# Performance work log

Hardware: AMD Instinct MI355X
Metric: run time of the kernel (lower is better)

The kernel has to match this reference:

```python
import jax, jax.numpy as jnp
import numpy as np

N_NODES = 100000
N_EDGES = 1600000
IN_FEATS = 128
OUT_FEATS = 48


def setup_inputs() -> dict:
    key = jax.random.key(0)
    ks = jax.random.split(key, 6)
    features = jax.random.normal(ks[0], (N_NODES, IN_FEATS), dtype=jnp.float32)
    # xavier_uniform for W.weight [out, in]
    lim_w = float(np.sqrt(6.0 / (IN_FEATS + OUT_FEATS)))
    W_w = jax.random.uniform(ks[1], (OUT_FEATS, IN_FEATS), dtype=jnp.float32, minval=-lim_w, maxval=lim_w)
    W_b = jnp.zeros((OUT_FEATS,), dtype=jnp.float32)
    # xavier_uniform for attn_w [2*out, 1]
    lim_a = float(np.sqrt(6.0 / (2 * OUT_FEATS + 1)))
    attn_w = jax.random.uniform(ks[2], (2 * OUT_FEATS, 1), dtype=jnp.float32, minval=-lim_a, maxval=lim_a)
    attn_b = jnp.zeros((1,), dtype=jnp.float32)
    src = jax.random.randint(ks[3], (N_EDGES,), 0, N_NODES, dtype=jnp.int32)
    dst = jax.random.randint(ks[4], (N_EDGES,), 0, N_NODES, dtype=jnp.int32)
    return {"features": features, "W_w": W_w, "W_b": W_b,
            "attn_w": attn_w, "attn_b": attn_b, "src": src, "dst": dst}


def reference(features, W_w, W_b, attn_w, attn_b, src, dst):
    n = features.shape[0]
    d = W_w.shape[0]
    # h = W(features)  [N, d]
    h = features @ W_w.T + W_b
    # cat([h[src], h[dst]]) @ attn_w == h[src] @ w_src + h[dst] @ w_dst
    w_src = attn_w[:d, 0]   # [d]
    w_dst = attn_w[d:, 0]   # [d]
    s_src = h @ w_src       # [N]
    s_dst = h @ w_dst       # [N]
    e = s_src[src] + s_dst[dst] + attn_b[0]            # [E]
    e = jax.nn.leaky_relu(e, negative_slope=0.2)
    # edge softmax grouped by destination node
    m = jax.ops.segment_max(e, dst, num_segments=n)     # [N]
    ex = jnp.exp(e - m[dst])                            # [E]
    denom = jax.ops.segment_sum(ex, dst, num_segments=n)  # [N]
    alpha = ex / denom[dst]                             # [E]
    # weighted scatter-sum: out[v] = sum_{(u,v) in E} alpha * h[u]
    msgs = h[src] * alpha[:, None]                      # [E, d]
    out = jax.ops.segment_sum(msgs, dst, num_segments=n)  # [N, d]
    return out
```

## Files before the change

kernel.cpp:

```cpp
#include <hip/hip_runtime.h>

#define NFEAT 128
#define DOUT 48
#define BSH 6
#define BNODES 64
#define PCAP 192
#define BCAP (PCAP * 8)
#define EPT 16
#define NBMAX 1568

typedef __attribute__((ext_vector_type(8))) short bf16x8;
typedef __attribute__((ext_vector_type(4))) float f32x4;

__device__ __forceinline__ float bf_lo(unsigned u) { return __uint_as_float(u << 16); }
__device__ __forceinline__ float bf_hi(unsigned u) { return __uint_as_float(u & 0xFFFF0000u); }
__device__ __forceinline__ unsigned bf_pack(float a, float b) {
    unsigned ua = __float_as_uint(a), ub = __float_as_uint(b);
    ua = (ua + 0x7FFFu + ((ua >> 16) & 1u)) >> 16;
    ub = (ub + 0x7FFFu + ((ub >> 16) & 1u)) & 0xFFFF0000u;
    return ua | ub;
}

__device__ __forceinline__ void split2(float x, short& hi, short& lo) {
    unsigned u = __float_as_uint(x);
    unsigned h = u & 0xFFFF0000u;
    hi = (short)(h >> 16);
    float r = x - __uint_as_float(h);
    unsigned v = __float_as_uint(r);
    lo = (short)((v + 0x7FFFu + ((v >> 16) & 1u)) >> 16);
}

__global__ __launch_bounds__(256) void k_proj(
    const float* __restrict__ feat, const float* __restrict__ Ww,
    const float* __restrict__ Wb, const float* __restrict__ attn_w,
    unsigned* __restrict__ hbf, float* __restrict__ s_src, float* __restrict__ s_dst,
    int n)
{
    __shared__ float hb[128][49];

    int tid  = threadIdx.x;
    int lane = tid & 63;
    int wv   = tid >> 6;
    int g    = lane >> 4;
    int r16  = lane & 15;

    int mbase = blockIdx.x * 128 + wv * 32;
    int na0 = mbase + r16;       if (na0 >= n) na0 = n - 1;
    int na1 = mbase + 16 + r16;  if (na1 >= n) na1 = n - 1;

    const float* fA0 = feat + (size_t)na0 * NFEAT + g * 4;
    const float* fA1 = feat + (size_t)na1 * NFEAT + g * 4;
    const float* wB  = Ww + (size_t)r16 * NFEAT + g * 4;

    f32x4 acc[2][3];
#pragma unroll
    for (int mt = 0; mt < 2; ++mt)
#pragma unroll
        for (int nt = 0; nt < 3; ++nt)
            acc[mt][nt] = (f32x4){0.f, 0.f, 0.f, 0.f};

#pragma unroll
    for (int ks = 0; ks < 4; ++ks) {
        f32x4 ra[4], rb[6];
        ra[0] = *(const f32x4*)(fA0 + ks * 32);
        ra[1] = *(const f32x4*)(fA0 + ks * 32 + 16);
        ra[2] = *(const f32x4*)(fA1 + ks * 32);
        ra[3] = *(const f32x4*)(fA1 + ks * 32 + 16);
        rb[0] = *(const f32x4*)(wB + ks * 32);
        rb[1] = *(const f32x4*)(wB + ks * 32 + 16);
        rb[2] = *(const f32x4*)(wB + 16 * NFEAT + ks * 32);
        rb[3] = *(const f32x4*)(wB + 16 * NFEAT + ks * 32 + 16);
        rb[4] = *(const f32x4*)(wB + 32 * NFEAT + ks * 32);
        rb[5] = *(const f32x4*)(wB + 32 * NFEAT + ks * 32 + 16);

        bf16x8 Ah[2], Al[2], Bh[3], Bl[3];
#pragma unroll
        for (int t = 0; t < 2; ++t) {
#pragma unroll
            for (int i = 0; i < 4; ++i) {
                short h, l;
                split2(ra[2 * t][i], h, l);     Ah[t][i] = h;     Al[t][i] = l;
                split2(ra[2 * t + 1][i], h, l); Ah[t][i + 4] = h; Al[t][i + 4] = l;
            }
        }
#pragma unroll
        for (int t = 0; t < 3; ++t) {
#pragma unroll
            for (int i = 0; i < 4; ++i) {
                short h, l;
                split2(rb[2 * t][i], h, l);     Bh[t][i] = h;     Bl[t][i] = l;
                split2(rb[2 * t + 1][i], h, l); Bh[t][i + 4] = h; Bl[t][i + 4] = l;
            }
        }
#pragma unroll
        for (int mt = 0; mt < 2; ++mt)
#pragma unroll
            for (int nt = 0; nt < 3; ++nt) {
                acc[mt][nt] = __builtin_amdgcn_mfma_f32_16x16x32_bf16(Ah[mt], Bh[nt], acc[mt][nt], 0, 0, 0);
                acc[mt][nt] = __builtin_amdgcn_mfma_f32_16x16x32_bf16(Al[mt], Bh[nt], acc[mt][nt], 0, 0, 0);
                acc[mt][nt] = __builtin_amdgcn_mfma_f32_16x16x32_bf16(Ah[mt], Bl[nt], acc[mt][nt], 0, 0, 0);
            }
    }

#pragma unroll
    for (int mt = 0; mt < 2; ++mt)
#pragma unroll
        for (int nt = 0; nt < 3; ++nt)
#pragma unroll
            for (int rr = 0; rr < 4; ++rr)
                hb[wv * 32 + mt * 16 + 4 * g + rr][nt * 16 + r16] = acc[mt][nt][rr];
    __syncthreads();

    int node = tid >> 1, part = tid & 1, jb = part * 24;
    int gn = blockIdx.x * 128 + node;
    float v[24];
    float ss = 0.f, sd = 0.f;
#pragma unroll
    for (int j = 0; j < 24; ++j) {
        float x = hb[node][jb + j] + Wb[jb + j];
        v[j] = x;
        ss = fmaf(x, attn_w[jb + j], ss);
        sd = fmaf(x, attn_w[DOUT + jb + j], sd);
    }
    ss += __shfl_xor(ss, 1, 64);
    sd += __shfl_xor(sd, 1, 64);

    if (gn < n) {
        uint4* hp = (uint4*)(hbf + (size_t)gn * 24 + part * 12);
#pragma unroll
        for (int q = 0; q < 3; ++q) {
            uint4 u;
            u.x = bf_pack(v[8 * q + 0], v[8 * q + 1]);
            u.y = bf_pack(v[8 * q + 2], v[8 * q + 3]);
            u.z = bf_pack(v[8 * q + 4], v[8 * q + 5]);
            u.w = bf_pack(v[8 * q + 6], v[8 * q + 7]);
            hp[q] = u;
        }
        if (part == 0) {
            s_src[gn] = ss;
            s_dst[gn] = sd;
        }
    }
}

__global__ __launch_bounds__(256) void k_bin(
    const int4* __restrict__ src4, const int4* __restrict__ dst4,
    const float* __restrict__ s_src, const float* __restrict__ s_dst,
    const float* __restrict__ attn_b,
    int* __restrict__ cursor, int2* __restrict__ ents, int nE, int NB)
{
    __shared__ int hist[NBMAX];
    __shared__ int bas[NBMAX];

    int tid = threadIdx.x;
    int cls = blockIdx.x & 7;
    long long e0 = (long long)blockIdx.x * 4096 + (long long)tid * EPT;

    for (int t = tid; t < NB; t += 256) hist[t] = 0;
    __syncthreads();

    int s[EPT], d[EPT];
    bool any = (e0 < nE);
#pragma unroll
    for (int q = 0; q < EPT / 4; ++q) {
        int4 sv = any ? src4[e0 / 4 + q] : make_int4(0, 0, 0, 0);
        int4 dv = any ? dst4[e0 / 4 + q] : make_int4(0, 0, 0, 0);
        s[4 * q + 0] = sv.x; s[4 * q + 1] = sv.y; s[4 * q + 2] = sv.z; s[4 * q + 3] = sv.w;
        d[4 * q + 0] = dv.x; d[4 * q + 1] = dv.y; d[4 * q + 2] = dv.z; d[4 * q + 3] = dv.w;
    }

    float vs[EPT], vd[EPT];
#pragma unroll
    for (int u = 0; u < EPT; ++u) vs[u] = s_src[s[u]];
#pragma unroll
    for (int u = 0; u < EPT; ++u) vd[u] = s_dst[d[u]];

    int rank[EPT];
#pragma unroll
    for (int u = 0; u < EPT; ++u)
        rank[u] = (e0 + u < nE) ? atomicAdd(&hist[d[u] >> BSH], 1) : 0;
    __syncthreads();

    for (int t = tid; t < NB; t += 256) {
        int c = hist[t];
        if (c > 0) bas[t] = atomicAdd(cursor + cls * NB + t, c);
    }
    __syncthreads();

    float ab = attn_b[0];
#pragma unroll
    for (int u = 0; u < EPT; ++u) {
        if (e0 + u < nE) {
            float v = vs[u] + vd[u] + ab;
            v = (v > 0.f) ? v : 0.2f * v;
            float x = __expf(v);
            int bkt = d[u] >> BSH;
            int slot = bas[bkt] + rank[u];
            if (slot < PCAP)
                ents[(size_t)bkt * BCAP + cls * PCAP + slot] =
                    make_int2(s[u] | ((d[u] & (BNODES - 1)) << 17), __float_as_int(x));
        }
    }
}

__global__ __launch_bounds__(256) void k_aggb(
    const unsigned* __restrict__ hbf, const int* __restrict__ cursor,
    const int2* __restrict__ ents, float* __restrict__ out, int n, int NB)
{
    __shared__ int2 se[BCAP];
    __shared__ unsigned short sidx[BCAP];
    __shared__ int c1[BNODES], c2[BNODES], lrp[BNODES + 1];
    __shared__ int cp[9];

    int b = blockIdx.x;
    int tid = threadIdx.x;

    if (tid < BNODES) { c1[tid] = 0; c2[tid] = 0; }
    __syncthreads();
    if (tid == 0) {
        int r = 0;
        for (int c = 0; c < 8; ++c) {
            cp[c] = r;
            r += min(cursor[c * NB + b], PCAP);
        }
        cp[8] = r;
    }
    __syncthreads();
    int total = cp[8];

    for (int i = tid; i < total; i += 256) {
        int c = 0;
        while (i >= cp[c + 1]) ++c;
        int2 v = ents[(size_t)b * BCAP + c * PCAP + (i - cp[c])];
        se[i] = v;
        atomicAdd(&c1[((unsigned)v.x) >> 17], 1);
    }
    __syncthreads();

    if (tid < BNODES) {
        int v = c1[tid];
        int p = v;
#pragma unroll
        for (int o = 1; o < 64; o <<= 1) {
            int u = __shfl_up(p, o, 64);
            if (tid >= o) p += u;
        }
        lrp[tid] = p - v;
        if (tid == BNODES - 1) lrp[BNODES] = p;
    }
    __syncthreads();

    for (int i = tid; i < total; i += 256) {
        int dl = ((unsigned)se[i].x) >> 17;
        int pos = lrp[dl] + atomicAdd(&c2[dl], 1);
        sidx[pos] = (unsigned short)i;
    }
    __syncthreads();

    int wave = tid >> 6, lane = tid & 63;
    int g = lane >> 3, sub = lane & 7;
    for (int dl = wave; dl < BNODES; dl += 4) {
        int node = (b << BSH) + dl;
        if (node >= n) break;
        int st = lrp[dl], en = lrp[dl + 1];
        float a0 = 0.f, a1 = 0.f, a2 = 0.f, a3 = 0.f, a4 = 0.f, a5 = 0.f, den = 0.f;
        for (int k = st + g; k < en; k += 8) {
            int2 ed = se[sidx[k]];
            float x = __int_as_float(ed.y);
            den += x;
            const unsigned* hr = hbf + (size_t)(ed.x & 0x1FFFF) * 24 + sub * 3;
            unsigned u0 = hr[0], u1 = hr[1], u2 = hr[2];
            a0 = fmaf(x, bf_lo(u0), a0);
            a1 = fmaf(x, bf_hi(u0), a1);
            a2 = fmaf(x, bf_lo(u1), a2);
            a3 = fmaf(x, bf_hi(u1), a3);
            a4 = fmaf(x, bf_lo(u2), a4);
            a5 = fmaf(x, bf_hi(u2), a5);
        }
#pragma unroll
        for (int o = 8; o <= 32; o <<= 1) {
            a0  += __shfl_xor(a0, o, 64);
            a1  += __shfl_xor(a1, o, 64);
            a2  += __shfl_xor(a2, o, 64);
            a3  += __shfl_xor(a3, o, 64);
            a4  += __shfl_xor(a4, o, 64);
            a5  += __shfl_xor(a5, o, 64);
            den += __shfl_xor(den, o, 64);
        }
        if (lane < 8) {
            float inv = (en > st) ? 1.f / den : 0.f;
            float* op = out + (size_t)node * DOUT + sub * 6;
            op[0] = a0 * inv;
            op[1] = a1 * inv;
            op[2] = a2 * inv;
            op[3] = a3 * inv;
            op[4] = a4 * inv;
            op[5] = a5 * inv;
        }
    }
}

extern "C" void kernel_launch(void* const* d_in, const int* in_sizes, int n_in,
                              void* d_out, int out_size, void* d_ws, size_t ws_size,
                              hipStream_t stream) {
    const float* feat   = (const float*)d_in[0];
    const float* Ww     = (const float*)d_in[1];
    const float* Wb     = (const float*)d_in[2];
    const float* attn_w = (const float*)d_in[3];
    const float* attn_b = (const float*)d_in[4];
    const int*   src    = (const int*)d_in[5];
    const int*   dst    = (const int*)d_in[6];

    int n  = in_sizes[0] / NFEAT;
    int nE = in_sizes[5];
    int NB = (n + BNODES - 1) / BNODES;
    int N8 = NB * 8;
    float* out = (float*)d_out;

    unsigned* hbf  = (unsigned*)d_ws;
    float* s_src   = (float*)(hbf + (size_t)n * 24);
    float* s_dst   = s_src + n;
    int*   cursor  = (int*)(s_dst + n);
    int2*  ents    = (int2*)(cursor + N8);

    hipMemsetAsync(cursor, 0, (size_t)N8 * sizeof(int), stream);

    int NBp = (n + 127) / 128;
    k_proj<<<NBp, 256, 0, stream>>>(feat, Ww, Wb, attn_w, hbf, s_src, s_dst, n);
    int nbb = (nE + 4095) / 4096;
    k_bin<<<nbb, 256, 0, stream>>>((const int4*)src, (const int4*)dst,
                                   s_src, s_dst, attn_b, cursor, ents, nE, NB);
    k_aggb<<<NB, 256, 0, stream>>>(hbf, cursor, ents, out, n, NB);
}
```

Before: 193.3 us.

## Pad bf16 h rows to 128B, widen aggregation block, sort edges directly

Pads each bf16 node row in the projected feature buffer from 96 to 128 bytes so every gathered row starts on a cache-line boundary. The aggregation kernel moves to 512 threads with 8 waves sharing the 64 destination nodes, and replaces the computed prefix over class counts with a shuffle scan. It stores sorted edge records directly instead of an index indirection, and unrolls the gather loop by two for more loads in flight. In exchange it uses more workspace and LDS (a second int2 array), which may lower occupancy.

```diff
diff --git a/kernel.cpp b/kernel.cpp
--- a/kernel.cpp
+++ b/kernel.cpp
@@ -8,6 +8,7 @@
 #define BCAP (PCAP * 8)
 #define EPT 16
 #define NBMAX 1568
+#define HSTRIDE 32
 
 typedef __attribute__((ext_vector_type(8))) short bf16x8;
 typedef __attribute__((ext_vector_type(4))) float f32x4;
@@ -126,7 +127,7 @@
     sd += __shfl_xor(sd, 1, 64);
 
     if (gn < n) {
-        uint4* hp = (uint4*)(hbf + (size_t)gn * 24 + part * 12);
+        uint4* hp = (uint4*)(hbf + (size_t)gn * HSTRIDE + part * 12);
 #pragma unroll
         for (int q = 0; q < 3; ++q) {
             uint4 u;
@@ -203,12 +204,12 @@
     }
 }
 
-__global__ __launch_bounds__(256) void k_aggb(
+__global__ __launch_bounds__(512) void k_aggb(
     const unsigned* __restrict__ hbf, const int* __restrict__ cursor,
     const int2* __restrict__ ents, float* __restrict__ out, int n, int NB)
 {
     __shared__ int2 se[BCAP];
-    __shared__ unsigned short sidx[BCAP];
+    __shared__ int2 sse[BCAP];
     __shared__ int c1[BNODES], c2[BNODES], lrp[BNODES + 1];
     __shared__ int cp[9];
 
@@ -216,19 +217,21 @@
     int tid = threadIdx.x;
 
     if (tid < BNODES) { c1[tid] = 0; c2[tid] = 0; }
-    __syncthreads();
-    if (tid == 0) {
-        int r = 0;
-        for (int c = 0; c < 8; ++c) {
-            cp[c] = r;
-            r += min(cursor[c * NB + b], PCAP);
-        }
-        cp[8] = r;
+    if (tid < 8) {
+        int c = min(cursor[tid * NB + b], PCAP);
+        int p = c;
+#pragma unroll
+        for (int o = 1; o < 8; o <<= 1) {
+            int u = __shfl_up(p, o, 64);
+            if (tid >= o) p += u;
+        }
+        cp[tid + 1] = p;
+        if (tid == 0) cp[0] = 0;
     }
     __syncthreads();
     int total = cp[8];
 
-    for (int i = tid; i < total; i += 256) {
+    for (int i = tid; i < total; i += 512) {
         int c = 0;
         while (i >= cp[c + 1]) ++c;
         int2 v = ents[(size_t)b * BCAP + c * PCAP + (i - cp[c])];
@@ -250,25 +253,49 @@
     }
     __syncthreads();
 
-    for (int i = tid; i < total; i += 256) {
-        int dl = ((unsigned)se[i].x) >> 17;
+    for (int i = tid; i < total; i += 512) {
+        int2 v = se[i];
+        int dl = ((unsigned)v.x) >> 17;
         int pos = lrp[dl] + atomicAdd(&c2[dl], 1);
-        sidx[pos] = (unsigned short)i;
+        sse[pos] = v;
     }
     __syncthreads();
 
     int wave = tid >> 6, lane = tid & 63;
     int g = lane >> 3, sub = lane & 7;
-    for (int dl = wave; dl < BNODES; dl += 4) {
+    for (int dl = wave; dl < BNODES; dl += 8) {
         int node = (b << BSH) + dl;
         if (node >= n) break;
         int st = lrp[dl], en = lrp[dl + 1];
         float a0 = 0.f, a1 = 0.f, a2 = 0.f, a3 = 0.f, a4 = 0.f, a5 = 0.f, den = 0.f;
-        for (int k = st + g; k < en; k += 8) {
-            int2 ed = se[sidx[k]];
+        int k = st + g;
+        for (; k + 8 < en; k += 16) {
+            int2 e1 = sse[k];
+            int2 e2 = sse[k + 8];
+            const unsigned* h1 = hbf + (size_t)(e1.x & 0x1FFFF) * HSTRIDE + sub * 3;
+            const unsigned* h2 = hbf + (size_t)(e2.x & 0x1FFFF) * HSTRIDE + sub * 3;
+            unsigned u10 = h1[0], u11 = h1[1], u12 = h1[2];
+            unsigned u20 = h2[0], u21 = h2[1], u22 = h2[2];
+            float x1 = __int_as_float(e1.y), x2 = __int_as_float(e2.y);
+            den += x1; den += x2;
+            a0 = fmaf(x1, bf_lo(u10), a0);
+            a1 = fmaf(x1, bf_hi(u10), a1);
+            a2 = fmaf(x1, bf_lo(u11), a2);
+            a3 = fmaf(x1, bf_hi(u11), a3);
+            a4 = fmaf(x1, bf_lo(u12), a4);
+            a5 = fmaf(x1, bf_hi(u12), a5);
+            a0 = fmaf(x2, bf_lo(u20), a0);
+            a1 = fmaf(x2, bf_hi(u20), a1);
+            a2 = fmaf(x2, bf_lo(u21), a2);
+            a3 = fmaf(x2, bf_hi(u21), a3);
+            a4 = fmaf(x2, bf_lo(u22), a4);
+            a5 = fmaf(x2, bf_hi(u22), a5);
+        }
+        if (k < en) {
+            int2 ed = sse[k];
             float x = __int_as_float(ed.y);
             den += x;
-            const unsigned* hr = hbf + (size_t)(ed.x & 0x1FFFF) * 24 + sub * 3;
+            const unsigned* hr = hbf + (size_t)(ed.x & 0x1FFFF) * HSTRIDE + sub * 3;
             unsigned u0 = hr[0], u1 = hr[1], u2 = hr[2];
             a0 = fmaf(x, bf_lo(u0), a0);
             a1 = fmaf(x, bf_hi(u0), a1);
@@ -318,7 +345,7 @@
     float* out = (float*)d_out;
 
     unsigned* hbf  = (unsigned*)d_ws;
-    float* s_src   = (float*)(hbf + (size_t)n * 24);
+    float* s_src   = (float*)(hbf + (size_t)n * HSTRIDE);
     float* s_dst   = s_src + n;
     int*   cursor  = (int*)(s_dst + n);
     int2*  ents    = (int2*)(cursor + N8);
@@ -330,5 +357,5 @@
     int nbb = (nE + 4095) / 4096;
     k_bin<<<nbb, 256, 0, stream>>>((const int4*)src, (const int4*)dst,
                                    s_src, s_dst, attn_b, cursor, ents, nE, NB);
-    k_aggb<<<NB, 256, 0, stream>>>(hbf, cursor, ents, out, n, NB);
-}
+    k_aggb<<<NB, 512, 0, stream>>>(hbf, cursor, ents, out, n, NB);
+}
```

Result: faster. 187.3 us (-3.1%).
